# Performance work log

Hardware: AMD Instinct MI355X
Metric: run time of the kernel (lower is better)

## Reference

```python
import jax, jax.numpy as jnp
import numpy as np

H = 2048        # hidden_size
NH = 32         # num_heads
HD = H // NH    # head_dim = 64
S = 512         # seq_len
UP = 2          # upsample_ratio
SU = S * UP     # upsampled seq len = 1024
INTER = 5632    # GatedMLP intermediate: int(2048*4*2/3) rounded up to mult of 256
EPS = 1e-6
DEPTH = 1


def rmsnorm(x, w):
    var = jnp.mean(jnp.square(x), axis=-1, keepdims=True)
    return x * jax.lax.rsqrt(var + EPS) * w


def setup_inputs() -> dict:
    key = jax.random.key(0)
    ks = jax.random.split(key, 12)
    sc = 0.02
    return {
        "hidden_states": jax.random.normal(ks[0], (2, S, H), dtype=jnp.float32),
        "W_up": jax.random.normal(ks[1], (SU, S), dtype=jnp.float32) * sc,
        "b_up": jnp.zeros((SU,), dtype=jnp.float32),
        "attn_norm_w": jnp.ones((H,), dtype=jnp.float32),
        "Wq": jax.random.normal(ks[2], (H, H), dtype=jnp.float32) * sc,
        "Wk": jax.random.normal(ks[3], (H, H), dtype=jnp.float32) * sc,
        "Wv": jax.random.normal(ks[4], (H, H), dtype=jnp.float32) * sc,
        "Wo": jax.random.normal(ks[5], (H, H), dtype=jnp.float32) * sc,
        "mlp_norm_w": jnp.ones((H,), dtype=jnp.float32),
        "Wg": jax.random.normal(ks[6], (INTER, H), dtype=jnp.float32) * sc,
        "Wu": jax.random.normal(ks[7], (INTER, H), dtype=jnp.float32) * sc,
        "Wd": jax.random.normal(ks[8], (H, INTER), dtype=jnp.float32) * sc,
    }


def reference(hidden_states, W_up, b_up, attn_norm_w, Wq, Wk, Wv, Wo,
              mlp_norm_w, Wg, Wu, Wd):
    B = hidden_states.shape[0]
    # init_upsampled_tokens: Linear over the sequence axis
    # up[b,t,d] = sum_s h[b,s,d] * W_up[t,s] + b_up[t]
    up = jnp.einsum('bsd,ts->btd', hidden_states, W_up) + b_up[None, :, None]

    for _ in range(DEPTH):
        residual = jnp.concatenate([hidden_states, up], axis=-2)  # [B, S+SU, H]
        x = rmsnorm(up, attn_norm_w)                               # [B, SU, H]
        q = (x @ Wq.T).reshape(B, SU, NH, HD)
        k = (residual @ Wk.T).reshape(B, S + SU, NH, HD)
        v = (residual @ Wv.T).reshape(B, S + SU, NH, HD)
        # explicit (non-causal) cross-attention, full score matrix
        scores = jnp.einsum('bshd,bthd->bsht', q, k) / np.sqrt(HD).astype(np.float32)
        attn = jax.nn.softmax(scores, axis=-1)
        o = jnp.einsum('bsht,bthd->bshd', attn, v).reshape(B, SU, H)
        x = (o @ Wo.T) + x                 # residual onto the *normed* tokens
        x = rmsnorm(x, mlp_norm_w)
        mlp_out = (jax.nn.silu(x @ Wg.T) * (x @ Wu.T)) @ Wd.T
        up = mlp_out + x
    return up
```

## Files before the change

### kernel.cpp

```cpp
#include <hip/hip_runtime.h>

typedef __bf16 bf16;
typedef __bf16 bf16x8 __attribute__((ext_vector_type(8)));
typedef float  f32x4  __attribute__((ext_vector_type(4)));
typedef unsigned int u32x4 __attribute__((ext_vector_type(4)));

#define NB 2
#define SS 512
#define HH 2048
#define SUx 1024
#define TT 1536
#define INTERx 5632

__device__ __forceinline__ void gload16(const bf16* g, bf16* l)
{
    __builtin_amdgcn_global_load_lds(
        (const __attribute__((address_space(1))) void*)g,
        (__attribute__((address_space(3))) void*)l, 16, 0, 0);
}

__global__ __launch_bounds__(256)
void cast_k(const float* __restrict__ in, bf16* __restrict__ out, long n)
{
    long i = ((long)blockIdx.x * 256 + threadIdx.x) * 8;
    if (i >= n) return;
    f32x4 a = *(const f32x4*)(in + i);
    f32x4 b = *(const f32x4*)(in + i + 4);
    bf16x8 o;
    o[0]=(bf16)a[0]; o[1]=(bf16)a[1]; o[2]=(bf16)a[2]; o[3]=(bf16)a[3];
    o[4]=(bf16)b[0]; o[5]=(bf16)b[1]; o[6]=(bf16)b[2]; o[7]=(bf16)b[3];
    *(bf16x8*)(out + i) = o;
}

template <typename TIN>
__global__ __launch_bounds__(256)
void transpose_k(const TIN* __restrict__ in, bf16* __restrict__ out,
                 int inRS, int outRS, int nz2,
                 long inZ1, long inZ2, long outZ1, long outZ2)
{
    __shared__ bf16 tile[64][65];
    int z1 = blockIdx.z / nz2, z2 = blockIdx.z % nz2;
    const TIN* ip = in + (long)z1*inZ1 + (long)z2*inZ2
                  + (long)blockIdx.x*64*inRS + (long)blockIdx.y*64;
    bf16* op = out + (long)z1*outZ1 + (long)z2*outZ2
             + (long)blockIdx.y*64*outRS + (long)blockIdx.x*64;
    int tc = threadIdx.x & 63, tr = threadIdx.x >> 6;
    #pragma unroll
    for (int rr = 0; rr < 64; rr += 4)
        tile[rr+tr][tc] = (bf16)(float)ip[(long)(rr+tr)*inRS + tc];
    __syncthreads();
    #pragma unroll
    for (int cc = 0; cc < 64; cc += 4)
        op[(long)(cc+tr)*outRS + tc] = tile[tc][cc+tr];
}

__global__ __launch_bounds__(256)
void rmsnorm_k(const float* __restrict__ x, const float* __restrict__ w,
               bf16* __restrict__ yb, float* __restrict__ yf)
{
    long row = blockIdx.x;
    const float* xp = x + row * HH;
    int t = threadIdx.x;
    f32x4 v0 = *(const f32x4*)(xp + t*8);
    f32x4 v1 = *(const f32x4*)(xp + t*8 + 4);
    float ss = 0.f;
    #pragma unroll
    for (int j = 0; j < 4; ++j) ss += v0[j]*v0[j] + v1[j]*v1[j];
    #pragma unroll
    for (int off = 32; off > 0; off >>= 1) ss += __shfl_xor(ss, off);
    __shared__ float red[4];
    if ((t & 63) == 0) red[t >> 6] = ss;
    __syncthreads();
    float tot = red[0] + red[1] + red[2] + red[3];
    float inv = rsqrtf(tot * (1.0f/(float)HH) + 1e-6f);
    f32x4 w0 = *(const f32x4*)(w + t*8);
    f32x4 w1 = *(const f32x4*)(w + t*8 + 4);
    f32x4 y0, y1; bf16x8 ob;
    #pragma unroll
    for (int j = 0; j < 4; ++j) {
        y0[j] = v0[j] * inv * w0[j];
        y1[j] = v1[j] * inv * w1[j];
        ob[j]   = (bf16)y0[j];
        ob[4+j] = (bf16)y1[j];
    }
    *(bf16x8*)(yb + row*HH + t*8) = ob;
    if (yf) {
        *(f32x4*)(yf + row*HH + t*8)     = y0;
        *(f32x4*)(yf + row*HH + t*8 + 4) = y1;
    }
}

__global__ __launch_bounds__(256)
void mul_k(bf16* __restrict__ g, const bf16* __restrict__ u, long n)
{
    long i = ((long)blockIdx.x * 256 + threadIdx.x) * 8;
    if (i >= n) return;
    bf16x8 a = *(const bf16x8*)(g + i);
    bf16x8 b = *(const bf16x8*)(u + i);
    bf16x8 o;
    #pragma unroll
    for (int j = 0; j < 8; ++j) o[j] = (bf16)((float)a[j] * (float)b[j]);
    *(bf16x8*)(g + i) = o;
}

__global__ __launch_bounds__(512)
void gemm_k(const bf16* __restrict__ A, const bf16* __restrict__ Bw,
            int Nsplit, int K,
            long sA, long sB,
            bf16* __restrict__ Cb, bf16* __restrict__ Cb2, long sCb,
            float* __restrict__ C32, long sC32,
            const float* __restrict__ res, long sRes,
            const float* __restrict__ bias,
            float scale, int doSilu)
{
    __shared__ alignas(16) bf16 As[2][128 * 64];
    __shared__ alignas(16) bf16 Bs[2][128 * 64];
    int z = blockIdx.z;
    const bf16* Ap = A  + (long)z * sA;
    const bf16* Bp = Bw + (long)z * sB;
    int n0 = blockIdx.x * 128, m0 = blockIdx.y * 128;
    int t = threadIdx.x, lane = t & 63, w = t >> 6;
    int wr = w >> 2, wc = w & 3;
    int lc = lane & 15, lg = lane >> 4;

    int lr = lane >> 3, ls = lane & 7;
    const bf16* gA[2]; const bf16* gB[2];
    int ldsOff[2];
    #pragma unroll
    for (int i = 0; i < 2; ++i) {
        int r = (i*8 + w)*8 + lr;
        int s = ls ^ lr;
        gA[i] = Ap + (long)(m0 + r) * K + s*8;
        gB[i] = Bp + (long)(n0 + r) * K + s*8;
        ldsOff[i] = (i*8 + w) * 512;
    }

    f32x4 zero = {0.f, 0.f, 0.f, 0.f};
    f32x4 acc[4][2];
    #pragma unroll
    for (int i = 0; i < 4; ++i)
        #pragma unroll
        for (int j = 0; j < 2; ++j) acc[i][j] = zero;

    int NKI = K >> 6;
    #pragma unroll
    for (int i = 0; i < 2; ++i) {
        gload16(gA[i], &As[0][0] + ldsOff[i]);
        gload16(gB[i], &Bs[0][0] + ldsOff[i]);
    }
    if (NKI > 1) {
        #pragma unroll
        for (int i = 0; i < 2; ++i) {
            gload16(gA[i] + 64, &As[1][0] + ldsOff[i]);
            gload16(gB[i] + 64, &Bs[1][0] + ldsOff[i]);
        }
    }

    for (int ks = 0; ks < NKI; ++ks) {
        int cur = ks & 1;
        const bf16* Asc = &As[cur][0];
        const bf16* Bsc = &Bs[cur][0];

        if (ks == NKI - 1) asm volatile("s_waitcnt vmcnt(0)" ::: "memory");
        else               asm volatile("s_waitcnt vmcnt(4)" ::: "memory");
        __builtin_amdgcn_s_barrier();
        __builtin_amdgcn_sched_barrier(0);

        #pragma unroll
        for (int kk = 0; kk < 2; ++kk) {
            bf16x8 af[4], bfv[2];
            #pragma unroll
            for (int i = 0; i < 4; ++i) {
                int rA = wr*64 + i*16 + lc;
                af[i]  = *(const bf16x8*)(Asc + rA*64 + (((kk*4 + lg) ^ (rA & 7)) * 8));
            }
            #pragma unroll
            for (int j = 0; j < 2; ++j) {
                int rB = wc*32 + j*16 + lc;
                bfv[j] = *(const bf16x8*)(Bsc + rB*64 + (((kk*4 + lg) ^ (rB & 7)) * 8));
            }
            __builtin_amdgcn_s_setprio(1);
            #pragma unroll
            for (int i = 0; i < 4; ++i)
                #pragma unroll
                for (int j = 0; j < 2; ++j)
                    acc[i][j] = __builtin_amdgcn_mfma_f32_16x16x32_bf16(af[i], bfv[j], acc[i][j], 0, 0, 0);
            __builtin_amdgcn_s_setprio(0);
        }

        __builtin_amdgcn_s_barrier();
        if (ks + 2 < NKI) {
            long ko = (long)(ks + 2) * 64;
            #pragma unroll
            for (int i = 0; i < 2; ++i) {
                gload16(gA[i] + ko, (bf16*)Asc + ldsOff[i]);
                gload16(gB[i] + ko, (bf16*)Bsc + ldsOff[i]);
            }
        }
    }

    #pragma unroll
    for (int i = 0; i < 4; ++i) {
        #pragma unroll
        for (int j = 0; j < 2; ++j) {
            int col = n0 + wc*32 + j*16 + lc;
            bf16* dst = Cb; int c2 = col;
            if (Cb2 && col >= Nsplit) { dst = Cb2; c2 = col - Nsplit; }
            int firstHalf = (col < Nsplit);
            #pragma unroll
            for (int r = 0; r < 4; ++r) {
                int row = m0 + wr*64 + i*16 + lg*4 + r;
                float v = acc[i][j][r] * scale;
                if (bias)   v += bias[row];
                if (doSilu && firstHalf) v = v / (1.f + __expf(-v));
                long off = (long)row * Nsplit + c2;
                if (res)  v += res[(long)z * sRes + off];
                if (C32)  C32[(long)z * sC32 + off] = v;
                if (dst)  dst[(long)z * sCb + off] = (bf16)v;
            }
        }
    }
}

__global__ __launch_bounds__(512)
void attn_k(const bf16* __restrict__ q, const bf16* __restrict__ k,
            const bf16* __restrict__ vt, bf16* __restrict__ o)
{
    int qc = blockIdx.x, h = blockIdx.y, b = blockIdx.z;
    int t = threadIdx.x, lane = t & 63, w = t >> 6;
    int lc = lane & 15, lg = lane >> 4;
    const bf16* qp = q  + ((long)(b*SUx + qc*256 + w*32)) * HH + h*64;
    const bf16* kp = k  + ((long)b*TT) * HH + h*64;
    const bf16* vp = vt + ((long)(b*32 + h)) * 64 * TT;

    __shared__ alignas(16) bf16 Ks[2][64*64];
    __shared__ alignas(16) bf16 Vs[2][64*64];
    __shared__ alignas(16) bf16 Ps[8][2][16*72];

    bf16x8 qf[2][2];
    #pragma unroll
    for (int s = 0; s < 2; ++s)
        #pragma unroll
        for (int kk = 0; kk < 2; ++kk)
            qf[s][kk] = *(const bf16x8*)(qp + (long)(s*16 + lc)*HH + kk*32 + lg*8);

    int lr = lane >> 3, ls = lane & 7;
    int srow = w*8 + lr;
    int sslot = ls ^ lr;
    const bf16* gK = kp + (long)srow * HH + sslot*8;
    const bf16* gV = vp + (long)srow * TT + sslot*8;
    int ldsO = w * 512;

    f32x4 zero = {0.f, 0.f, 0.f, 0.f};
    f32x4 oacc[2][4];
    float lsum[2][4];
    #pragma unroll
    for (int qs = 0; qs < 2; ++qs) {
        #pragma unroll
        for (int r = 0; r < 4; ++r) lsum[qs][r] = 0.f;
        #pragma unroll
        for (int dt = 0; dt < 4; ++dt) oacc[qs][dt] = zero;
    }

    const int NS = TT / 64;
    gload16(gK,            &Ks[0][0] + ldsO);
    gload16(gV,            &Vs[0][0] + ldsO);
    gload16(gK + 64L*HH,   &Ks[1][0] + ldsO);
    gload16(gV + 64,       &Vs[1][0] + ldsO);

    for (int st = 0; st < NS; ++st) {
        int cur = st & 1;
        const bf16* Kc = &Ks[cur][0];
        const bf16* Vc = &Vs[cur][0];

        if (st == NS - 1) asm volatile("s_waitcnt vmcnt(0)" ::: "memory");
        else              asm volatile("s_waitcnt vmcnt(2)" ::: "memory");
        __builtin_amdgcn_s_barrier();
        __builtin_amdgcn_sched_barrier(0);

        bf16x8 kf[4][2];
        #pragma unroll
        for (int s2 = 0; s2 < 4; ++s2) {
            int row = s2*16 + lc;
            #pragma unroll
            for (int kk = 0; kk < 2; ++kk)
                kf[s2][kk] = *(const bf16x8*)(Kc + row*64 + (((kk*4 + lg) ^ (row & 7)) * 8));
        }
        f32x4 sv[2][4];
        __builtin_amdgcn_s_setprio(1);
        #pragma unroll
        for (int qs = 0; qs < 2; ++qs)
            #pragma unroll
            for (int s2 = 0; s2 < 4; ++s2) {
                f32x4 a0 = __builtin_amdgcn_mfma_f32_16x16x32_bf16(qf[qs][0], kf[s2][0], zero, 0, 0, 0);
                sv[qs][s2] = __builtin_amdgcn_mfma_f32_16x16x32_bf16(qf[qs][1], kf[s2][1], a0, 0, 0, 0);
            }
        __builtin_amdgcn_s_setprio(0);

        bf16* Pw = &Ps[w][0][0];
        #pragma unroll
        for (int qs = 0; qs < 2; ++qs)
            #pragma unroll
            for (int r = 0; r < 4; ++r) {
                int prow = lg*4 + r;
                #pragma unroll
                for (int s2 = 0; s2 < 4; ++s2) {
                    float p = __expf(sv[qs][s2][r]);
                    lsum[qs][r] += p;
                    Pw[qs*(16*72) + prow*72 + s2*16 + lc] = (bf16)p;
                }
            }
        asm volatile("s_waitcnt lgkmcnt(0)" ::: "memory");
        __builtin_amdgcn_sched_barrier(0);

        bf16x8 pf[2][2];
        #pragma unroll
        for (int qs = 0; qs < 2; ++qs)
            #pragma unroll
            for (int ks = 0; ks < 2; ++ks)
                pf[qs][ks] = *(const bf16x8*)(Pw + qs*(16*72) + lc*72 + (ks*4 + lg)*8);
        bf16x8 vf[4][2];
        #pragma unroll
        for (int dt = 0; dt < 4; ++dt) {
            int row = dt*16 + lc;
            #pragma unroll
            for (int ks = 0; ks < 2; ++ks)
                vf[dt][ks] = *(const bf16x8*)(Vc + row*64 + (((ks*4 + lg) ^ (row & 7)) * 8));
        }
        __builtin_amdgcn_s_setprio(1);
        #pragma unroll
        for (int qs = 0; qs < 2; ++qs)
            #pragma unroll
            for (int dt = 0; dt < 4; ++dt) {
                oacc[qs][dt] = __builtin_amdgcn_mfma_f32_16x16x32_bf16(pf[qs][0], vf[dt][0], oacc[qs][dt], 0, 0, 0);
                oacc[qs][dt] = __builtin_amdgcn_mfma_f32_16x16x32_bf16(pf[qs][1], vf[dt][1], oacc[qs][dt], 0, 0, 0);
            }
        __builtin_amdgcn_s_setprio(0);

        __builtin_amdgcn_s_barrier();
        if (st + 2 < NS) {
            long t2 = (long)(st + 2) * 64;
            gload16(gK + t2*HH, (bf16*)Kc + ldsO);
            gload16(gV + t2,    (bf16*)Vc + ldsO);
        }
    }

    #pragma unroll
    for (int qs = 0; qs < 2; ++qs)
        #pragma unroll
        for (int r = 0; r < 4; ++r) {
            float l = lsum[qs][r];
            l += __shfl_xor(l, 1);
            l += __shfl_xor(l, 2);
            l += __shfl_xor(l, 4);
            l += __shfl_xor(l, 8);
            float inv = 1.0f / l;
            long row = (long)b*SUx + qc*256 + w*32 + qs*16 + lg*4 + r;
            #pragma unroll
            for (int dt = 0; dt < 4; ++dt)
                o[row*HH + h*64 + dt*16 + lc] = (bf16)(oacc[qs][dt][r] * inv);
        }
}

extern "C" void kernel_launch(void* const* d_in, const int* in_sizes, int n_in,
                              void* d_out, int out_size, void* d_ws, size_t ws_size,
                              hipStream_t stream)
{
    const float* hs  = (const float*)d_in[0];
    const float* Wup = (const float*)d_in[1];
    const float* bup = (const float*)d_in[2];
    const float* anw = (const float*)d_in[3];
    const float* Wq  = (const float*)d_in[4];
    const float* Wk  = (const float*)d_in[5];
    const float* Wv  = (const float*)d_in[6];
    const float* Wo  = (const float*)d_in[7];
    const float* mnw = (const float*)d_in[8];
    const float* Wg  = (const float*)d_in[9];
    const float* Wu  = (const float*)d_in[10];
    const float* Wd  = (const float*)d_in[11];
    float* outp = (float*)d_out;

    char* p = (char*)d_ws;
    auto take = [&](size_t bytes) -> void* {
        void* r = (void*)p;
        p += (bytes + 255) & ~(size_t)255;
        return r;
    };

    bf16* wq  = (bf16*)take((size_t)HH*HH*2);
    bf16* wk  = (bf16*)take((size_t)HH*HH*2);
    bf16* wv  = (bf16*)take((size_t)HH*HH*2);
    bf16* wo  = (bf16*)take((size_t)HH*HH*2);
    bf16* wg  = (bf16*)take((size_t)INTERx*HH*2);
    bf16* wu  = (bf16*)take((size_t)INTERx*HH*2);
    bf16* wd  = (bf16*)take((size_t)INTERx*HH*2);
    bf16* wup = (bf16*)take((size_t)SUx*SS*2);
    bf16* ht  = (bf16*)take((size_t)NB*HH*SS*2);
    bf16* resb= (bf16*)take((size_t)NB*TT*HH*2);
    float* x1f= (float*)take((size_t)NB*SUx*HH*4);
    bf16* x1b = (bf16*)take((size_t)NB*SUx*HH*2);
    float* upf= (float*)take((size_t)NB*SUx*HH*4);

    size_t mlp_bytes = (size_t)NB*SUx*HH*4 + (size_t)NB*SUx*HH*2
                     + 2*(size_t)NB*SUx*INTERx*2;
    char* un = (char*)take(mlp_bytes);
    bf16* qb  = (bf16*)un;
    bf16* kb  = qb  + (size_t)NB*SUx*HH;
    bf16* vb  = kb  + (size_t)NB*TT*HH;
    bf16* vtb = vb  + (size_t)NB*TT*HH;
    bf16* ob  = vtb + (size_t)NB*TT*HH;
    float* x2f= (float*)un;
    bf16* x2b = (bf16*)(un + (size_t)NB*SUx*HH*4);
    bf16* gb  = x2b + (size_t)NB*SUx*HH;
    bf16* ub  = gb  + (size_t)NB*SUx*INTERx;

    cast_k<<<dim3((unsigned)((size_t)HH*HH/2048)), 256, 0, stream>>>(Wq, wq, (long)HH*HH);
    cast_k<<<dim3((unsigned)((size_t)HH*HH/2048)), 256, 0, stream>>>(Wk, wk, (long)HH*HH);
    cast_k<<<dim3((unsigned)((size_t)HH*HH/2048)), 256, 0, stream>>>(Wv, wv, (long)HH*HH);
    cast_k<<<dim3((unsigned)((size_t)HH*HH/2048)), 256, 0, stream>>>(Wo, wo, (long)HH*HH);
    cast_k<<<dim3((unsigned)((size_t)INTERx*HH/2048)), 256, 0, stream>>>(Wg, wg, (long)INTERx*HH);
    cast_k<<<dim3((unsigned)((size_t)INTERx*HH/2048)), 256, 0, stream>>>(Wu, wu, (long)INTERx*HH);
    cast_k<<<dim3((unsigned)((size_t)INTERx*HH/2048)), 256, 0, stream>>>(Wd, wd, (long)INTERx*HH);
    cast_k<<<dim3((unsigned)((size_t)SUx*SS/2048)), 256, 0, stream>>>(Wup, wup, (long)SUx*SS);
    for (int b = 0; b < NB; ++b)
        cast_k<<<dim3((unsigned)((size_t)SS*HH/2048)), 256, 0, stream>>>(
            hs + (size_t)b*SS*HH, resb + (size_t)b*TT*HH, (long)SS*HH);

    transpose_k<float><<<dim3(SS/64, HH/64, NB), 256, 0, stream>>>(
        hs, ht, HH, SS, 1, (long)SS*HH, 0, (long)HH*SS, 0);

    gemm_k<<<dim3(HH/128, SUx/128, NB), 512, 0, stream>>>(
        wup, ht, HH, SS, 0, (long)HH*SS,
        resb + (size_t)SS*HH, nullptr, (long)TT*HH,
        upf, (long)SUx*HH,
        nullptr, 0, bup, 1.0f, 0);

    rmsnorm_k<<<dim3(NB*SUx), 256, 0, stream>>>(upf, anw, x1b, x1f);

    gemm_k<<<dim3(HH/128, (NB*SUx)/128, 1), 512, 0, stream>>>(
        x1b, wq, HH, HH, 0, 0, qb, nullptr, 0, nullptr, 0, nullptr, 0, nullptr, 0.125f, 0);
    gemm_k<<<dim3((2*HH)/128, (NB*TT)/128, 1), 512, 0, stream>>>(
        resb, wk, HH, HH, 0, 0, kb, vb, 0, nullptr, 0, nullptr, 0, nullptr, 1.0f, 0);

    transpose_k<bf16><<<dim3(TT/64, 1, NB*32), 256, 0, stream>>>(
        vb, vtb, HH, TT, 32, (long)TT*HH, 64, (long)32*64*TT, (long)64*TT);

    attn_k<<<dim3(SUx/256, 32, NB), 512, 0, stream>>>(qb, kb, vtb, ob);

    gemm_k<<<dim3(HH/128, (NB*SUx)/128, 1), 512, 0, stream>>>(
        ob, wo, HH, HH, 0, 0, nullptr, nullptr, 0, upf, 0, x1f, 0, nullptr, 1.0f, 0);

    rmsnorm_k<<<dim3(NB*SUx), 256, 0, stream>>>(upf, mnw, x2b, x2f);

    gemm_k<<<dim3((2*INTERx)/128, (NB*SUx)/128, 1), 512, 0, stream>>>(
        x2b, wg, INTERx, HH, 0, 0, gb, ub, 0, nullptr, 0, nullptr, 0, nullptr, 1.0f, 1);
    mul_k<<<dim3((unsigned)((size_t)NB*SUx*INTERx/2048)), 256, 0, stream>>>(
        gb, ub, (long)NB*SUx*INTERx);

    gemm_k<<<dim3(HH/128, (NB*SUx)/128, 1), 512, 0, stream>>>(
        gb, wd, HH, INTERx, 0, 0, nullptr, nullptr, 0, outp, 0, x2f, 0, nullptr, 1.0f, 0);

    (void)in_sizes; (void)n_in; (void)out_size; (void)ws_size;
}
```

Baseline: 567.7 us.

## Read fp32 weights directly in GEMM, dropping separate bf16 cast kernels

Adds a template mode to the GEMM in which the B operand (the weights) is staged into LDS as fp32 and converted to bf16 in registers just before the MFMA. This removes five weight-cast kernels (Wq, Wk, Wv, Wo, Wd) and their extra read and write passes over global memory. The K/V GEMM now picks between Wk and Wv by column block. It also adds an XCD-aware remap of workgroup indices for L2 locality. The cost is twice the LDS for B, twice the global bytes for B inside the GEMMs, and extra per-iteration conversion work in the inner loop.

New measurement: 629.7 us. 1.11x slower.

```diff
diff --git a/kernel.cpp b/kernel.cpp
--- a/kernel.cpp
+++ b/kernel.cpp
@@ -12,7 +12,7 @@
 #define TT 1536
 #define INTERx 5632
 
-__device__ __forceinline__ void gload16(const bf16* g, bf16* l)
+__device__ __forceinline__ void gload16(const void* g, void* l)
 {
     __builtin_amdgcn_global_load_lds(
         (const __attribute__((address_space(1))) void*)g,
@@ -103,8 +103,10 @@
     *(bf16x8*)(g + i) = o;
 }
 
+template <int BF32>
 __global__ __launch_bounds__(512)
-void gemm_k(const bf16* __restrict__ A, const bf16* __restrict__ Bw,
+void gemm_k(const bf16* __restrict__ A,
+            const void* __restrict__ Bw, const void* __restrict__ Bw2,
             int Nsplit, int K,
             long sA, long sB,
             bf16* __restrict__ Cb, bf16* __restrict__ Cb2, long sCb,
@@ -114,25 +116,57 @@
             float scale, int doSilu)
 {
     __shared__ alignas(16) bf16 As[2][128 * 64];
-    __shared__ alignas(16) bf16 Bs[2][128 * 64];
+    __shared__ alignas(16) bf16 Bs[2][128 * 64 * (BF32 ? 2 : 1)];
     int z = blockIdx.z;
-    const bf16* Ap = A  + (long)z * sA;
-    const bf16* Bp = Bw + (long)z * sB;
-    int n0 = blockIdx.x * 128, m0 = blockIdx.y * 128;
+    const bf16* Ap = A + (long)z * sA;
+
+    int gx = gridDim.x;
+    int nwg = gx * gridDim.y;
+    int lin = blockIdx.y * gx + blockIdx.x;
+    int qq = nwg >> 3, r8 = nwg & 7;
+    int xcd = lin & 7, off = lin >> 3;
+    int wg = (xcd < r8 ? xcd * (qq + 1) : r8 * (qq + 1) + (xcd - r8) * qq) + off;
+    int n0 = (wg % gx) * 128, m0 = (wg / gx) * 128;
+
     int t = threadIdx.x, lane = t & 63, w = t >> 6;
     int wr = w >> 2, wc = w & 3;
     int lc = lane & 15, lg = lane >> 4;
 
     int lr = lane >> 3, ls = lane & 7;
-    const bf16* gA[2]; const bf16* gB[2];
-    int ldsOff[2];
+    const bf16* gA[2];
+    int ldsOffA[2];
     #pragma unroll
     for (int i = 0; i < 2; ++i) {
         int r = (i*8 + w)*8 + lr;
-        int s = ls ^ lr;
-        gA[i] = Ap + (long)(m0 + r) * K + s*8;
-        gB[i] = Bp + (long)(n0 + r) * K + s*8;
-        ldsOff[i] = (i*8 + w) * 512;
+        gA[i] = Ap + (long)(m0 + r) * K + (ls ^ lr) * 8;
+        ldsOffA[i] = (i*8 + w) * 512;
+    }
+
+    const bf16*  gBh[2];  int ldsOffBh[2];
+    const float* gBf[4];  int ldsOffBf[4];
+    if (BF32) {
+        const float* B1 = (const float*)Bw;
+        const float* B2 = (const float*)Bw2;
+        const float* BpF; long nrow0;
+        if (!Bw2 || n0 < Nsplit) { BpF = B1 + (long)z * sB; nrow0 = n0; }
+        else                     { BpF = B2;                nrow0 = n0 - Nsplit; }
+        int lrB = lane >> 4, lsB = lane & 15;
+        #pragma unroll
+        for (int i = 0; i < 4; ++i) {
+            int r = i*32 + w*4 + lrB;
+            int pd = lsB >> 1, hf = lsB & 1;
+            int ps = pd ^ (r & 7);
+            gBf[i] = BpF + (long)(nrow0 + r) * K + ps*8 + hf*4;
+            ldsOffBf[i] = (i*32 + w*4) * 64;
+        }
+    } else {
+        const bf16* Bp = (const bf16*)Bw + (long)z * sB;
+        #pragma unroll
+        for (int i = 0; i < 2; ++i) {
+            int r = (i*8 + w)*8 + lr;
+            gBh[i] = Bp + (long)(n0 + r) * K + (ls ^ lr) * 8;
+            ldsOffBh[i] = (i*8 + w) * 512;
+        }
     }
 
     f32x4 zero = {0.f, 0.f, 0.f, 0.f};
@@ -142,27 +176,33 @@
         #pragma unroll
         for (int j = 0; j < 2; ++j) acc[i][j] = zero;
 
+    auto stage = [&](int buf, int ti) {
+        long ko = (long)ti * 64;
+        #pragma unroll
+        for (int i = 0; i < 2; ++i)
+            gload16(gA[i] + ko, &As[buf][0] + ldsOffA[i]);
+        if (BF32) {
+            #pragma unroll
+            for (int i = 0; i < 4; ++i)
+                gload16(gBf[i] + ko, (float*)&Bs[buf][0] + ldsOffBf[i]);
+        } else {
+            #pragma unroll
+            for (int i = 0; i < 2; ++i)
+                gload16(gBh[i] + ko, &Bs[buf][0] + ldsOffBh[i]);
+        }
+    };
+
     int NKI = K >> 6;
-    #pragma unroll
-    for (int i = 0; i < 2; ++i) {
-        gload16(gA[i], &As[0][0] + ldsOff[i]);
-        gload16(gB[i], &Bs[0][0] + ldsOff[i]);
-    }
-    if (NKI > 1) {
-        #pragma unroll
-        for (int i = 0; i < 2; ++i) {
-            gload16(gA[i] + 64, &As[1][0] + ldsOff[i]);
-            gload16(gB[i] + 64, &Bs[1][0] + ldsOff[i]);
-        }
-    }
+    stage(0, 0);
+    if (NKI > 1) stage(1, 1);
 
     for (int ks = 0; ks < NKI; ++ks) {
         int cur = ks & 1;
         const bf16* Asc = &As[cur][0];
-        const bf16* Bsc = &Bs[cur][0];
-
-        if (ks == NKI - 1) asm volatile("s_waitcnt vmcnt(0)" ::: "memory");
-        else               asm volatile("s_waitcnt vmcnt(4)" ::: "memory");
+
+        if (ks == NKI - 1)  asm volatile("s_waitcnt vmcnt(0)" ::: "memory");
+        else if (BF32)      asm volatile("s_waitcnt vmcnt(6)" ::: "memory");
+        else                asm volatile("s_waitcnt vmcnt(4)" ::: "memory");
         __builtin_amdgcn_s_barrier();
         __builtin_amdgcn_sched_barrier(0);
 
@@ -174,10 +214,27 @@
                 int rA = wr*64 + i*16 + lc;
                 af[i]  = *(const bf16x8*)(Asc + rA*64 + (((kk*4 + lg) ^ (rA & 7)) * 8));
             }
-            #pragma unroll
-            for (int j = 0; j < 2; ++j) {
-                int rB = wc*32 + j*16 + lc;
-                bfv[j] = *(const bf16x8*)(Bsc + rB*64 + (((kk*4 + lg) ^ (rB & 7)) * 8));
+            if (BF32) {
+                const float* Bq = (const float*)&Bs[cur][0];
+                #pragma unroll
+                for (int j = 0; j < 2; ++j) {
+                    int rB = wc*32 + j*16 + lc;
+                    int pr = (kk*4 + lg) ^ (rB & 7);
+                    f32x4 b0 = *(const f32x4*)(Bq + (long)rB*64 + pr*8);
+                    f32x4 b1 = *(const f32x4*)(Bq + (long)rB*64 + pr*8 + 4);
+                    #pragma unroll
+                    for (int e = 0; e < 4; ++e) {
+                        bfv[j][e]   = (bf16)b0[e];
+                        bfv[j][4+e] = (bf16)b1[e];
+                    }
+                }
+            } else {
+                const bf16* Bsc = &Bs[cur][0];
+                #pragma unroll
+                for (int j = 0; j < 2; ++j) {
+                    int rB = wc*32 + j*16 + lc;
+                    bfv[j] = *(const bf16x8*)(Bsc + rB*64 + (((kk*4 + lg) ^ (rB & 7)) * 8));
+                }
             }
             __builtin_amdgcn_s_setprio(1);
             #pragma unroll
@@ -189,14 +246,7 @@
         }
 
         __builtin_amdgcn_s_barrier();
-        if (ks + 2 < NKI) {
-            long ko = (long)(ks + 2) * 64;
-            #pragma unroll
-            for (int i = 0; i < 2; ++i) {
-                gload16(gA[i] + ko, (bf16*)Asc + ldsOff[i]);
-                gload16(gB[i] + ko, (bf16*)Bsc + ldsOff[i]);
-            }
-        }
+        if (ks + 2 < NKI) stage(cur, ks + 2);
     }
 
     #pragma unroll
@@ -387,13 +437,8 @@
         return r;
     };
 
-    bf16* wq  = (bf16*)take((size_t)HH*HH*2);
-    bf16* wk  = (bf16*)take((size_t)HH*HH*2);
-    bf16* wv  = (bf16*)take((size_t)HH*HH*2);
-    bf16* wo  = (bf16*)take((size_t)HH*HH*2);
-    bf16* wg  = (bf16*)take((size_t)INTERx*HH*2);
-    bf16* wu  = (bf16*)take((size_t)INTERx*HH*2);
-    bf16* wd  = (bf16*)take((size_t)INTERx*HH*2);
+    bf16* wg  = (bf16*)take(2 * (size_t)INTERx*HH*2);
+    bf16* wu  = wg + (size_t)INTERx*HH;
     bf16* wup = (bf16*)take((size_t)SUx*SS*2);
     bf16* ht  = (bf16*)take((size_t)NB*HH*SS*2);
     bf16* resb= (bf16*)take((size_t)NB*TT*HH*2);
@@ -414,13 +459,8 @@
     bf16* gb  = x2b + (size_t)NB*SUx*HH;
     bf16* ub  = gb  + (size_t)NB*SUx*INTERx;
 
-    cast_k<<<dim3((unsigned)((size_t)HH*HH/2048)), 256, 0, stream>>>(Wq, wq, (long)HH*HH);
-    cast_k<<<dim3((unsigned)((size_t)HH*HH/2048)), 256, 0, stream>>>(Wk, wk, (long)HH*HH);
-    cast_k<<<dim3((unsigned)((size_t)HH*HH/2048)), 256, 0, stream>>>(Wv, wv, (long)HH*HH);
-    cast_k<<<dim3((unsigned)((size_t)HH*HH/2048)), 256, 0, stream>>>(Wo, wo, (long)HH*HH);
     cast_k<<<dim3((unsigned)((size_t)INTERx*HH/2048)), 256, 0, stream>>>(Wg, wg, (long)INTERx*HH);
     cast_k<<<dim3((unsigned)((size_t)INTERx*HH/2048)), 256, 0, stream>>>(Wu, wu, (long)INTERx*HH);
-    cast_k<<<dim3((unsigned)((size_t)INTERx*HH/2048)), 256, 0, stream>>>(Wd, wd, (long)INTERx*HH);
     cast_k<<<dim3((unsigned)((size_t)SUx*SS/2048)), 256, 0, stream>>>(Wup, wup, (long)SUx*SS);
     for (int b = 0; b < NB; ++b)
         cast_k<<<dim3((unsigned)((size_t)SS*HH/2048)), 256, 0, stream>>>(
@@ -429,36 +469,36 @@
     transpose_k<float><<<dim3(SS/64, HH/64, NB), 256, 0, stream>>>(
         hs, ht, HH, SS, 1, (long)SS*HH, 0, (long)HH*SS, 0);
 
-    gemm_k<<<dim3(HH/128, SUx/128, NB), 512, 0, stream>>>(
-        wup, ht, HH, SS, 0, (long)HH*SS,
+    gemm_k<0><<<dim3(HH/128, SUx/128, NB), 512, 0, stream>>>(
+        wup, ht, nullptr, HH, SS, 0, (long)HH*SS,
         resb + (size_t)SS*HH, nullptr, (long)TT*HH,
         upf, (long)SUx*HH,
         nullptr, 0, bup, 1.0f, 0);
 
     rmsnorm_k<<<dim3(NB*SUx), 256, 0, stream>>>(upf, anw, x1b, x1f);
 
-    gemm_k<<<dim3(HH/128, (NB*SUx)/128, 1), 512, 0, stream>>>(
-        x1b, wq, HH, HH, 0, 0, qb, nullptr, 0, nullptr, 0, nullptr, 0, nullptr, 0.125f, 0);
-    gemm_k<<<dim3((2*HH)/128, (NB*TT)/128, 1), 512, 0, stream>>>(
-        resb, wk, HH, HH, 0, 0, kb, vb, 0, nullptr, 0, nullptr, 0, nullptr, 1.0f, 0);
+    gemm_k<1><<<dim3(HH/128, (NB*SUx)/128, 1), 512, 0, stream>>>(
+        x1b, Wq, nullptr, HH, HH, 0, 0, qb, nullptr, 0, nullptr, 0, nullptr, 0, nullptr, 0.125f, 0);
+    gemm_k<1><<<dim3((2*HH)/128, (NB*TT)/128, 1), 512, 0, stream>>>(
+        resb, Wk, Wv, HH, HH, 0, 0, kb, vb, 0, nullptr, 0, nullptr, 0, nullptr, 1.0f, 0);
 
     transpose_k<bf16><<<dim3(TT/64, 1, NB*32), 256, 0, stream>>>(
         vb, vtb, HH, TT, 32, (long)TT*HH, 64, (long)32*64*TT, (long)64*TT);
 
     attn_k<<<dim3(SUx/256, 32, NB), 512, 0, stream>>>(qb, kb, vtb, ob);
 
-    gemm_k<<<dim3(HH/128, (NB*SUx)/128, 1), 512, 0, stream>>>(
-        ob, wo, HH, HH, 0, 0, nullptr, nullptr, 0, upf, 0, x1f, 0, nullptr, 1.0f, 0);
+    gemm_k<1><<<dim3(HH/128, (NB*SUx)/128, 1), 512, 0, stream>>>(
+        ob, Wo, nullptr, HH, HH, 0, 0, nullptr, nullptr, 0, upf, 0, x1f, 0, nullptr, 1.0f, 0);
 
     rmsnorm_k<<<dim3(NB*SUx), 256, 0, stream>>>(upf, mnw, x2b, x2f);
 
-    gemm_k<<<dim3((2*INTERx)/128, (NB*SUx)/128, 1), 512, 0, stream>>>(
-        x2b, wg, INTERx, HH, 0, 0, gb, ub, 0, nullptr, 0, nullptr, 0, nullptr, 1.0f, 1);
+    gemm_k<0><<<dim3((2*INTERx)/128, (NB*SUx)/128, 1), 512, 0, stream>>>(
+        x2b, wg, nullptr, INTERx, HH, 0, 0, gb, ub, 0, nullptr, 0, nullptr, 0, nullptr, 1.0f, 1);
     mul_k<<<dim3((unsigned)((size_t)NB*SUx*INTERx/2048)), 256, 0, stream>>>(
         gb, ub, (long)NB*SUx*INTERx);
 
-    gemm_k<<<dim3(HH/128, (NB*SUx)/128, 1), 512, 0, stream>>>(
-        gb, wd, HH, INTERx, 0, 0, nullptr, nullptr, 0, outp, 0, x2f, 0, nullptr, 1.0f, 0);
+    gemm_k<1><<<dim3(HH/128, (NB*SUx)/128, 1), 512, 0, stream>>>(
+        gb, Wd, nullptr, HH, INTERx, 0, 0, nullptr, nullptr, 0, outp, 0, x2f, 0, nullptr, 1.0f, 0);
 
     (void)in_sizes; (void)n_in; (void)out_size; (void)ws_size;
 }
```

## Fuse SiLU-gate multiply into interleaved gate/up GEMM and remap workgroups per XCD

Applied to the files above, without the earlier changes.

The gate/up GEMM now loads interleaved rows of Wg and Wu, so each pair of adjacent output columns holds a gate and an up value. Lanes exchange these pairs with a shuffle and write silu(g)*u straight out, which removes the separate mul_k pass and the extra intermediate buffer. All GEMMs also remap the linear block id so that consecutive tiles go to the same XCD, aiming for better L2 reuse. The cost is half the lanes sitting idle during the epilogue stores, plus strided bf16 writes of the product.

Result: faster. 535.9 us (-5.6%).

```diff
diff --git a/kernel.cpp b/kernel.cpp
--- a/kernel.cpp
+++ b/kernel.cpp
@@ -12,7 +12,7 @@
 #define TT 1536
 #define INTERx 5632
 
-__device__ __forceinline__ void gload16(const bf16* g, bf16* l)
+__device__ __forceinline__ void gload16(const void* g, void* l)
 {
     __builtin_amdgcn_global_load_lds(
         (const __attribute__((address_space(1))) void*)g,
@@ -90,19 +90,7 @@
     }
 }
 
-__global__ __launch_bounds__(256)
-void mul_k(bf16* __restrict__ g, const bf16* __restrict__ u, long n)
-{
-    long i = ((long)blockIdx.x * 256 + threadIdx.x) * 8;
-    if (i >= n) return;
-    bf16x8 a = *(const bf16x8*)(g + i);
-    bf16x8 b = *(const bf16x8*)(u + i);
-    bf16x8 o;
-    #pragma unroll
-    for (int j = 0; j < 8; ++j) o[j] = (bf16)((float)a[j] * (float)b[j]);
-    *(bf16x8*)(g + i) = o;
-}
-
+template <int GU>
 __global__ __launch_bounds__(512)
 void gemm_k(const bf16* __restrict__ A, const bf16* __restrict__ Bw,
             int Nsplit, int K,
@@ -116,9 +104,16 @@
     __shared__ alignas(16) bf16 As[2][128 * 64];
     __shared__ alignas(16) bf16 Bs[2][128 * 64];
     int z = blockIdx.z;
-    const bf16* Ap = A  + (long)z * sA;
-    const bf16* Bp = Bw + (long)z * sB;
-    int n0 = blockIdx.x * 128, m0 = blockIdx.y * 128;
+    const bf16* Ap = A + (long)z * sA;
+
+    int gx = gridDim.x;
+    int nwg = gx * gridDim.y;
+    int lin = blockIdx.y * gx + blockIdx.x;
+    int qq = nwg >> 3, r8 = nwg & 7;
+    int xcd = lin & 7, off = lin >> 3;
+    int wg = (xcd < r8 ? xcd * (qq + 1) : r8 * (qq + 1) + (xcd - r8) * qq) + off;
+    int n0 = (wg % gx) * 128, m0 = (wg / gx) * 128;
+
     int t = threadIdx.x, lane = t & 63, w = t >> 6;
     int wr = w >> 2, wc = w & 3;
     int lc = lane & 15, lg = lane >> 4;
@@ -129,9 +124,14 @@
     #pragma unroll
     for (int i = 0; i < 2; ++i) {
         int r = (i*8 + w)*8 + lr;
-        int s = ls ^ lr;
-        gA[i] = Ap + (long)(m0 + r) * K + s*8;
-        gB[i] = Bp + (long)(n0 + r) * K + s*8;
+        gA[i] = Ap + (long)(m0 + r) * K + (ls ^ lr) * 8;
+        if (GU) {
+            long grow = (long)(n0 >> 1) + (r >> 1);
+            gB[i] = Bw + ((r & 1) ? (long)INTERx * K : 0) + grow * K + (ls ^ lr) * 8;
+        } else {
+            const bf16* Bp = Bw + (long)z * sB;
+            gB[i] = Bp + (long)(n0 + r) * K + (ls ^ lr) * 8;
+        }
         ldsOff[i] = (i*8 + w) * 512;
     }
 
@@ -199,24 +199,46 @@
         }
     }
 
-    #pragma unroll
-    for (int i = 0; i < 4; ++i) {
-        #pragma unroll
-        for (int j = 0; j < 2; ++j) {
-            int col = n0 + wc*32 + j*16 + lc;
-            bf16* dst = Cb; int c2 = col;
-            if (Cb2 && col >= Nsplit) { dst = Cb2; c2 = col - Nsplit; }
-            int firstHalf = (col < Nsplit);
-            #pragma unroll
-            for (int r = 0; r < 4; ++r) {
-                int row = m0 + wr*64 + i*16 + lg*4 + r;
-                float v = acc[i][j][r] * scale;
-                if (bias)   v += bias[row];
-                if (doSilu && firstHalf) v = v / (1.f + __expf(-v));
-                long off = (long)row * Nsplit + c2;
-                if (res)  v += res[(long)z * sRes + off];
-                if (C32)  C32[(long)z * sC32 + off] = v;
-                if (dst)  dst[(long)z * sCb + off] = (bf16)v;
+    if (GU) {
+        #pragma unroll
+        for (int i = 0; i < 4; ++i) {
+            #pragma unroll
+            for (int j = 0; j < 2; ++j) {
+                int tc2 = wc*32 + j*16 + lc;
+                int colp = (n0 >> 1) + (tc2 >> 1);
+                #pragma unroll
+                for (int r = 0; r < 4; ++r) {
+                    int row = m0 + wr*64 + i*16 + lg*4 + r;
+                    float v = acc[i][j][r];
+                    float pv = __shfl_xor(v, 1);
+                    float g  = (lc & 1) ? pv : v;
+                    float uu = (lc & 1) ? v  : pv;
+                    float prod = (g / (1.f + __expf(-g))) * uu;
+                    if (!(lc & 1))
+                        Cb[(long)row * Nsplit + colp] = (bf16)prod;
+                }
+            }
+        }
+    } else {
+        #pragma unroll
+        for (int i = 0; i < 4; ++i) {
+            #pragma unroll
+            for (int j = 0; j < 2; ++j) {
+                int col = n0 + wc*32 + j*16 + lc;
+                bf16* dst = Cb; int c2 = col;
+                if (Cb2 && col >= Nsplit) { dst = Cb2; c2 = col - Nsplit; }
+                int firstHalf = (col < Nsplit);
+                #pragma unroll
+                for (int r = 0; r < 4; ++r) {
+                    int row = m0 + wr*64 + i*16 + lg*4 + r;
+                    float v = acc[i][j][r] * scale;
+                    if (bias)   v += bias[row];
+                    if (doSilu && firstHalf) v = v / (1.f + __expf(-v));
+                    long off = (long)row * Nsplit + c2;
+                    if (res)  v += res[(long)z * sRes + off];
+                    if (C32)  C32[(long)z * sC32 + off] = v;
+                    if (dst)  dst[(long)z * sCb + off] = (bf16)v;
+                }
             }
         }
     }
@@ -388,11 +410,10 @@
     };
 
     bf16* wq  = (bf16*)take((size_t)HH*HH*2);
-    bf16* wk  = (bf16*)take((size_t)HH*HH*2);
-    bf16* wv  = (bf16*)take((size_t)HH*HH*2);
+    bf16* wk  = (bf16*)take(2 * (size_t)HH*HH*2);
+    bf16* wv  = wk + (size_t)HH*HH;
     bf16* wo  = (bf16*)take((size_t)HH*HH*2);
-    bf16* wg  = (bf16*)take((size_t)INTERx*HH*2);
-    bf16* wu  = (bf16*)take((size_t)INTERx*HH*2);
+    bf16* wgu = (bf16*)take(2 * (size_t)INTERx*HH*2);
     bf16* wd  = (bf16*)take((size_t)INTERx*HH*2);
     bf16* wup = (bf16*)take((size_t)SUx*SS*2);
     bf16* ht  = (bf16*)take((size_t)NB*HH*SS*2);
@@ -401,9 +422,9 @@
     bf16* x1b = (bf16*)take((size_t)NB*SUx*HH*2);
     float* upf= (float*)take((size_t)NB*SUx*HH*4);
 
-    size_t mlp_bytes = (size_t)NB*SUx*HH*4 + (size_t)NB*SUx*HH*2
-                     + 2*(size_t)NB*SUx*INTERx*2;
-    char* un = (char*)take(mlp_bytes);
+    size_t attn_bytes = (size_t)NB*SUx*HH*2 + 3*(size_t)NB*TT*HH*2 + (size_t)NB*SUx*HH*2;
+    size_t mlp_bytes  = (size_t)NB*SUx*HH*4 + (size_t)NB*SUx*HH*2 + (size_t)NB*SUx*INTERx*2;
+    char* un = (char*)take(attn_bytes > mlp_bytes ? attn_bytes : mlp_bytes);
     bf16* qb  = (bf16*)un;
     bf16* kb  = qb  + (size_t)NB*SUx*HH;
     bf16* vb  = kb  + (size_t)NB*TT*HH;
@@ -412,14 +433,13 @@
     float* x2f= (float*)un;
     bf16* x2b = (bf16*)(un + (size_t)NB*SUx*HH*4);
     bf16* gb  = x2b + (size_t)NB*SUx*HH;
-    bf16* ub  = gb  + (size_t)NB*SUx*INTERx;
 
     cast_k<<<dim3((unsigned)((size_t)HH*HH/2048)), 256, 0, stream>>>(Wq, wq, (long)HH*HH);
     cast_k<<<dim3((unsigned)((size_t)HH*HH/2048)), 256, 0, stream>>>(Wk, wk, (long)HH*HH);
     cast_k<<<dim3((unsigned)((size_t)HH*HH/2048)), 256, 0, stream>>>(Wv, wv, (long)HH*HH);
     cast_k<<<dim3((unsigned)((size_t)HH*HH/2048)), 256, 0, stream>>>(Wo, wo, (long)HH*HH);
-    cast_k<<<dim3((unsigned)((size_t)INTERx*HH/2048)), 256, 0, stream>>>(Wg, wg, (long)INTERx*HH);
-    cast_k<<<dim3((unsigned)((size_t)INTERx*HH/2048)), 256, 0, stream>>>(Wu, wu, (long)INTERx*HH);
+    cast_k<<<dim3((unsigned)((size_t)INTERx*HH/2048)), 256, 0, stream>>>(Wg, wgu, (long)INTERx*HH);
+    cast_k<<<dim3((unsigned)((size_t)INTERx*HH/2048)), 256, 0, stream>>>(Wu, wgu + (size_t)INTERx*HH, (long)INTERx*HH);
     cast_k<<<dim3((unsigned)((size_t)INTERx*HH/2048)), 256, 0, stream>>>(Wd, wd, (long)INTERx*HH);
     cast_k<<<dim3((unsigned)((size_t)SUx*SS/2048)), 256, 0, stream>>>(Wup, wup, (long)SUx*SS);
     for (int b = 0; b < NB; ++b)
@@ -429,7 +449,7 @@
     transpose_k<float><<<dim3(SS/64, HH/64, NB), 256, 0, stream>>>(
         hs, ht, HH, SS, 1, (long)SS*HH, 0, (long)HH*SS, 0);
 
-    gemm_k<<<dim3(HH/128, SUx/128, NB), 512, 0, stream>>>(
+    gemm_k<0><<<dim3(HH/128, SUx/128, NB), 512, 0, stream>>>(
         wup, ht, HH, SS, 0, (long)HH*SS,
         resb + (size_t)SS*HH, nullptr, (long)TT*HH,
         upf, (long)SUx*HH,
@@ -437,9 +457,9 @@
 
     rmsnorm_k<<<dim3(NB*SUx), 256, 0, stream>>>(upf, anw, x1b, x1f);
 
-    gemm_k<<<dim3(HH/128, (NB*SUx)/128, 1), 512, 0, stream>>>(
+    gemm_k<0><<<dim3(HH/128, (NB*SUx)/128, 1), 512, 0, stream>>>(
         x1b, wq, HH, HH, 0, 0, qb, nullptr, 0, nullptr, 0, nullptr, 0, nullptr, 0.125f, 0);
-    gemm_k<<<dim3((2*HH)/128, (NB*TT)/128, 1), 512, 0, stream>>>(
+    gemm_k<0><<<dim3((2*HH)/128, (NB*TT)/128, 1), 512, 0, stream>>>(
         resb, wk, HH, HH, 0, 0, kb, vb, 0, nullptr, 0, nullptr, 0, nullptr, 1.0f, 0);
 
     transpose_k<bf16><<<dim3(TT/64, 1, NB*32), 256, 0, stream>>>(
@@ -447,17 +467,15 @@
 
     attn_k<<<dim3(SUx/256, 32, NB), 512, 0, stream>>>(qb, kb, vtb, ob);
 
-    gemm_k<<<dim3(HH/128, (NB*SUx)/128, 1), 512, 0, stream>>>(
+    gemm_k<0><<<dim3(HH/128, (NB*SUx)/128, 1), 512, 0, stream>>>(
         ob, wo, HH, HH, 0, 0, nullptr, nullptr, 0, upf, 0, x1f, 0, nullptr, 1.0f, 0);
 
     rmsnorm_k<<<dim3(NB*SUx), 256, 0, stream>>>(upf, mnw, x2b, x2f);
 
-    gemm_k<<<dim3((2*INTERx)/128, (NB*SUx)/128, 1), 512, 0, stream>>>(
-        x2b, wg, INTERx, HH, 0, 0, gb, ub, 0, nullptr, 0, nullptr, 0, nullptr, 1.0f, 1);
-    mul_k<<<dim3((unsigned)((size_t)NB*SUx*INTERx/2048)), 256, 0, stream>>>(
-        gb, ub, (long)NB*SUx*INTERx);
-
-    gemm_k<<<dim3(HH/128, (NB*SUx)/128, 1), 512, 0, stream>>>(
+    gemm_k<1><<<dim3((2*INTERx)/128, (NB*SUx)/128, 1), 512, 0, stream>>>(
+        x2b, wgu, INTERx, HH, 0, 0, gb, nullptr, 0, nullptr, 0, nullptr, 0, nullptr, 1.0f, 0);
+
+    gemm_k<0><<<dim3(HH/128, (NB*SUx)/128, 1), 512, 0, stream>>>(
         gb, wd, HH, INTERx, 0, 0, nullptr, nullptr, 0, outp, 0, x2f, 0, nullptr, 1.0f, 0);
 
     (void)in_sizes; (void)n_in; (void)out_size; (void)ws_size;
```
